# Performance work log

Hardware: AMD Instinct MI355X
Metric: run time of the kernel (lower is better)

The kernel has to match this reference:

```python
import jax, jax.numpy as jnp
import numpy as np

B, N, D = 2, 2048, 1024
H, DH = 16, 64
INNER = H * DH  # 1024
EPS = 1e-5


def setup_inputs() -> dict:
    key = jax.random.key(0)
    ks = jax.random.split(key, 7)
    x = jax.random.normal(ks[0], (B, N, D), dtype=jnp.float32)
    mask = jax.random.uniform(ks[1], (B, N)) < 0.9
    mask = mask.at[:, 0].set(True)  # guarantee at least one valid key per row
    attn_bias = jax.random.normal(ks[2], (H, N, N), dtype=jnp.float32) * 0.02
    ln_w = jnp.ones((D,), dtype=jnp.float32)
    ln_b = jnp.zeros((D,), dtype=jnp.float32)
    wq = jax.random.normal(ks[3], (D, INNER), dtype=jnp.float32) * 0.02
    wkv = jax.random.normal(ks[4], (D, 2 * DH), dtype=jnp.float32) * 0.02
    wo = jax.random.normal(ks[5], (INNER, D), dtype=jnp.float32) * 0.02
    return {"x": x, "attn_bias": attn_bias, "ln_w": ln_w, "ln_b": ln_b,
            "wq": wq, "wkv": wkv, "wo": wo, "mask": mask}


def reference(x, attn_bias, ln_w, ln_b, wq, wkv, wo, mask):
    scale = DH ** -0.5
    # NOTE: in the torch module, kv_input = x BEFORE self.norm (context=None),
    # so K/V come from raw x while Q comes from LayerNorm(x).
    mu = jnp.mean(x, axis=-1, keepdims=True)
    var = jnp.var(x, axis=-1, keepdims=True)
    xn = (x - mu) / jnp.sqrt(var + EPS) * ln_w + ln_b
    q = (xn @ wq).reshape(B, N, H, DH).transpose(0, 2, 1, 3) * scale  # b h n d
    kv = x @ wkv                     # b n 2*dh (shared single KV head, MQA)
    k, v = kv[..., :DH], kv[..., DH:]
    sim = jnp.einsum('bhid,bjd->bhij', q, k) + attn_bias  # bias broadcasts over b
    mask_value = -jnp.finfo(sim.dtype).max
    sim = jnp.where(mask[:, None, None, :], sim, mask_value)
    attn = jax.nn.softmax(sim, axis=-1)
    out = jnp.einsum('bhij,bjd->bhid', attn, v)
    out = out.transpose(0, 2, 1, 3).reshape(B, N, INNER)
    return out @ wo
```

## Files before the change

### kernel.cpp

```cpp
#include <hip/hip_runtime.h>
#include <hip/hip_bf16.h>

typedef __bf16 bf16_t;
typedef __bf16 bf16x4 __attribute__((ext_vector_type(4)));
typedef __bf16 bf16x8 __attribute__((ext_vector_type(8)));
typedef float f32x4 __attribute__((ext_vector_type(4)));

static constexpr int BB    = 2;
static constexpr int SEQ   = 2048;
static constexpr int DM    = 1024;
static constexpr int NHEAD = 16;
static constexpr int HD    = 64;
static constexpr float L2E = 1.4426950408889634f;

__device__ __forceinline__ bf16x8 ld8(const bf16_t* p) {
  return *reinterpret_cast<const bf16x8*>(p);
}

__device__ __forceinline__ void gl_lds16(const bf16_t* g, bf16_t* l) {
  __builtin_amdgcn_global_load_lds(
      (const __attribute__((address_space(1))) void*)g,
      (__attribute__((address_space(3))) void*)l, 16, 0, 0);
}

__device__ __forceinline__ uint2 shfl2(uint2 v, int src) {
  uint2 r;
  r.x = (unsigned)__shfl((int)v.x, src, 64);
  r.y = (unsigned)__shfl((int)v.y, src, 64);
  return r;
}

template <typename T> __device__ __forceinline__ T cvt_out(float v);
template <> __device__ __forceinline__ float  cvt_out<float >(float v) { return v; }
template <> __device__ __forceinline__ bf16_t cvt_out<bf16_t>(float v) { return (bf16_t)v; }

__global__ __launch_bounds__(256) void transpose_cast(const float* __restrict__ in,
                                                      bf16_t* __restrict__ out,
                                                      int R, int C) {
  __shared__ float tile[32][33];
  const int c0 = blockIdx.x * 32, r0 = blockIdx.y * 32;
  const int tx = threadIdx.x & 31, ty = threadIdx.x >> 5;
#pragma unroll
  for (int y = ty; y < 32; y += 8)
    tile[y][tx] = in[(size_t)(r0 + y) * C + (c0 + tx)];
  __syncthreads();
#pragma unroll
  for (int y = ty; y < 32; y += 8)
    out[(size_t)(c0 + y) * R + (r0 + tx)] = (bf16_t)tile[tx][y];
}

__global__ __launch_bounds__(256) void row_prep(const float* __restrict__ x,
    const float* __restrict__ ln_w, const float* __restrict__ ln_b,
    const int* __restrict__ mask,
    bf16_t* __restrict__ xbf, bf16_t* __restrict__ xn, float* __restrict__ maskA) {
  const int row = blockIdx.x, t = threadIdx.x;
  __shared__ float red[8];
  const float4 xv = *reinterpret_cast<const float4*>(&x[(size_t)row * DM + t * 4]);
  float s  = xv.x + xv.y + xv.z + xv.w;
  float s2 = xv.x * xv.x + xv.y * xv.y + xv.z * xv.z + xv.w * xv.w;
#pragma unroll
  for (int off = 32; off >= 1; off >>= 1) {
    s  += __shfl_xor(s,  off, 64);
    s2 += __shfl_xor(s2, off, 64);
  }
  if ((t & 63) == 0) { red[t >> 6] = s; red[4 + (t >> 6)] = s2; }
  __syncthreads();
  s  = red[0] + red[1] + red[2] + red[3];
  s2 = red[4] + red[5] + red[6] + red[7];
  const float mu   = s * (1.0f / DM);
  const float var  = s2 * (1.0f / DM) - mu * mu;
  const float rstd = rsqrtf(var + 1e-5f);
  const float4 wv = *reinterpret_cast<const float4*>(&ln_w[t * 4]);
  const float4 bv = *reinterpret_cast<const float4*>(&ln_b[t * 4]);
  union { bf16_t h[4]; uint2 u; } p0, p1;
  p0.h[0] = (bf16_t)xv.x; p0.h[1] = (bf16_t)xv.y;
  p0.h[2] = (bf16_t)xv.z; p0.h[3] = (bf16_t)xv.w;
  p1.h[0] = (bf16_t)((xv.x - mu) * rstd * wv.x + bv.x);
  p1.h[1] = (bf16_t)((xv.y - mu) * rstd * wv.y + bv.y);
  p1.h[2] = (bf16_t)((xv.z - mu) * rstd * wv.z + bv.z);
  p1.h[3] = (bf16_t)((xv.w - mu) * rstd * wv.w + bv.w);
  *reinterpret_cast<uint2*>(&xbf[(size_t)row * DM + t * 4]) = p0.u;
  *reinterpret_cast<uint2*>(&xn [(size_t)row * DM + t * 4]) = p1.u;
  if (t == 0) maskA[row] = mask[row] ? 0.0f : -1e30f;
}

__device__ __forceinline__ void gemm_core_db(
    const bf16_t* __restrict__ A, const bf16_t* __restrict__ Bt, int K,
    int m0, int n0, bf16_t* As, bf16_t* Bs, f32x4 (&acc)[4][4]) {
  const int t = threadIdx.x, lane = t & 63, w = t >> 6;
  const int wm = (w & 1) * 64, wn = (w >> 1) * 64;
  const int l15 = lane & 15, q4 = lane >> 4;
  const int sr = lane >> 2, sc = (lane & 3) * 8;
  const bf16_t* Ap0 = A  + (size_t)(m0 + w * 32 + sr) * K + sc;
  const bf16_t* Ap1 = Ap0 + (size_t)16 * K;
  const bf16_t* Bp0 = Bt + (size_t)(n0 + w * 32 + sr) * K + sc;
  const bf16_t* Bp1 = Bp0 + (size_t)16 * K;
  const int la0 = (w * 32) * 32, la1 = (w * 32 + 16) * 32;
  gl_lds16(Ap0, As + la0);
  gl_lds16(Ap1, As + la1);
  gl_lds16(Bp0, Bs + la0);
  gl_lds16(Bp1, Bs + la1);
  __syncthreads();
  int buf = 0;
  for (int k0 = 0; k0 < K; k0 += 32) {
    const int nbuf = buf ^ 1;
    if (k0 + 32 < K) {
      const int kn = k0 + 32;
      gl_lds16(Ap0 + kn, As + nbuf * (128 * 32) + la0);
      gl_lds16(Ap1 + kn, As + nbuf * (128 * 32) + la1);
      gl_lds16(Bp0 + kn, Bs + nbuf * (128 * 32) + la0);
      gl_lds16(Bp1 + kn, Bs + nbuf * (128 * 32) + la1);
    }
    const bf16_t* Asb = As + buf * (128 * 32);
    const bf16_t* Bsb = Bs + buf * (128 * 32);
    bf16x8 af[4], bfr[4];
#pragma unroll
    for (int mt = 0; mt < 4; ++mt) af[mt]  = ld8(&Asb[(wm + mt * 16 + l15) * 32 + q4 * 8]);
#pragma unroll
    for (int nt = 0; nt < 4; ++nt) bfr[nt] = ld8(&Bsb[(wn + nt * 16 + l15) * 32 + q4 * 8]);
#pragma unroll
    for (int mt = 0; mt < 4; ++mt)
#pragma unroll
      for (int nt = 0; nt < 4; ++nt)
        acc[mt][nt] = __builtin_amdgcn_mfma_f32_16x16x32_bf16(af[mt], bfr[nt], acc[mt][nt], 0, 0, 0);
    __syncthreads();
    buf = nbuf;
  }
}

__global__ __launch_bounds__(256) void gemm_qkv(
    const bf16_t* __restrict__ xn,  const bf16_t* __restrict__ wqT,  bf16_t* __restrict__ qb,
    const bf16_t* __restrict__ xbf, const bf16_t* __restrict__ wkvT,
    bf16_t* __restrict__ kkb, bf16_t* __restrict__ vTb) {
  __shared__ alignas(16) bf16_t As[2][128 * 32];
  __shared__ alignas(16) bf16_t Bs[2][128 * 32];
  const int bx = blockIdx.x;
  const bool isKV = (bx < 32);
  const int m0 = isKV ? bx * 128 : ((bx - 32) & 31) * 128;
  const int n0 = isKV ? 0 : ((bx - 32) >> 5) * 128;
  const bf16_t* A  = isKV ? xbf  : xn;
  const bf16_t* Bt = isKV ? wkvT : wqT;
  f32x4 acc[4][4] = {};
  gemm_core_db(A, Bt, DM, m0, n0, &As[0][0], &Bs[0][0], acc);

  const int lane = threadIdx.x & 63, w = threadIdx.x >> 6;
  const int wm = (w & 1) * 64, wn = (w >> 1) * 64;
  const int l15 = lane & 15, q4 = lane >> 4;
#pragma unroll
  for (int mt = 0; mt < 4; ++mt)
#pragma unroll
    for (int nt = 0; nt < 4; ++nt)
#pragma unroll
      for (int r = 0; r < 4; ++r) {
        const int gm = m0 + wm + mt * 16 + q4 * 4 + r;
        const int gn = n0 + wn + nt * 16 + l15;
        if (isKV) {
          const bf16_t ov = (bf16_t)acc[mt][nt][r];
          if (gn < HD) kkb[(size_t)gm * HD + gn] = ov;
          else vTb[((size_t)(gm >> 11) * HD + (gn - HD)) * SEQ + (gm & 2047)] = ov;
        } else {
          qb[(size_t)gm * DM + gn] = (bf16_t)(acc[mt][nt][r] * 0.125f);
        }
      }
}

__global__ __launch_bounds__(256) void gemm_out(const bf16_t* __restrict__ A,
    const bf16_t* __restrict__ Bt, float* __restrict__ C, int K) {
  __shared__ alignas(16) bf16_t As[2][128 * 32];
  __shared__ alignas(16) bf16_t Bs[2][128 * 32];
  const int m0 = blockIdx.x * 128, n0 = blockIdx.y * 128;
  f32x4 acc[4][4] = {};
  gemm_core_db(A, Bt, K, m0, n0, &As[0][0], &Bs[0][0], acc);
  const int lane = threadIdx.x & 63, w = threadIdx.x >> 6;
  const int wm = (w & 1) * 64, wn = (w >> 1) * 64;
  const int l15 = lane & 15, q4 = lane >> 4;
#pragma unroll
  for (int mt = 0; mt < 4; ++mt)
#pragma unroll
    for (int nt = 0; nt < 4; ++nt)
#pragma unroll
      for (int r = 0; r < 4; ++r) {
        const int gm = m0 + wm + mt * 16 + q4 * 4 + r;
        const int gn = n0 + wn + nt * 16 + l15;
        C[(size_t)gm * DM + gn] = acc[mt][nt][r];
      }
}

__global__ __launch_bounds__(256, 4) void flash_attn(
    const bf16_t* __restrict__ q,
    const bf16_t* __restrict__ kk,
    const bf16_t* __restrict__ vT,
    const float*  __restrict__ bias,
    const float*  __restrict__ maskA,
    bf16_t* __restrict__ aout)
{
  const int b = blockIdx.y & 1, h = blockIdx.y >> 1;
  const int i0 = blockIdx.x * 64;
  const int t = threadIdx.x, lane = t & 63, w = t >> 6;
  const int l15 = lane & 15, q4 = lane >> 4;

  __shared__ alignas(16) bf16_t Ks[2][64][72];
  __shared__ alignas(16) bf16_t Vs[2][64][72];

  const bf16_t* qrow = &q[((size_t)b * SEQ + i0 + w * 16 + l15) * DM + h * HD];
  const bf16x8 bq0 = ld8(qrow + q4 * 8);
  const bf16x8 bq1 = ld8(qrow + 32 + q4 * 8);

  f32x4 o[4] = {};
  float m_run = -1e30f, l_run = 0.0f;

  const float* bias_p = bias + (size_t)h * SEQ * SEQ
                      + (size_t)(i0 + w * 16 + l15) * SEQ + q4 * 4;
  const float* mask_p = maskA + b * SEQ + q4 * 4;

  const int sr = t >> 2, sc = (t & 3) * 16;
  const bf16_t* kp = &kk[((size_t)b * SEQ + sr) * HD + sc];
  const bf16_t* vp = &vT[((size_t)b * HD + sr) * SEQ + sc];

  uint4 kr0 = *reinterpret_cast<const uint4*>(kp);
  uint4 kr1 = *reinterpret_cast<const uint4*>(kp + 8);
  uint4 vr0 = *reinterpret_cast<const uint4*>(vp);
  uint4 vr1 = *reinterpret_cast<const uint4*>(vp + 8);
  f32x4 bm[4];
#pragma unroll
  for (int mt = 0; mt < 4; ++mt) {
    const f32x4 bv = *reinterpret_cast<const f32x4*>(bias_p + mt * 16);
    const f32x4 mv = *reinterpret_cast<const f32x4*>(mask_p + mt * 16);
    bm[mt] = bv + mv;
  }
  *reinterpret_cast<uint4*>(&Ks[0][sr][sc])     = kr0;
  *reinterpret_cast<uint4*>(&Ks[0][sr][sc + 8]) = kr1;
  *reinterpret_cast<uint4*>(&Vs[0][sr][sc])     = vr0;
  *reinterpret_cast<uint4*>(&Vs[0][sr][sc + 8]) = vr1;
  __syncthreads();

  for (int it = 0; it < SEQ / 64; ++it) {
    const int buf = it & 1;
    const int j1 = (it + 1) * 64;
    const bool more = (j1 < SEQ);
    if (more) {
      kr0 = *reinterpret_cast<const uint4*>(kp + (size_t)j1 * HD);
      kr1 = *reinterpret_cast<const uint4*>(kp + (size_t)j1 * HD + 8);
      vr0 = *reinterpret_cast<const uint4*>(vp + j1);
      vr1 = *reinterpret_cast<const uint4*>(vp + j1 + 8);
    }

    f32x4 s[4];
    __builtin_amdgcn_s_setprio(1);
#pragma unroll
    for (int mt = 0; mt < 4; ++mt) {
      const bf16x8 a0 = ld8(&Ks[buf][mt * 16 + l15][q4 * 8]);
      const bf16x8 a1 = ld8(&Ks[buf][mt * 16 + l15][32 + q4 * 8]);
      f32x4 z = {0.f, 0.f, 0.f, 0.f};
      z = __builtin_amdgcn_mfma_f32_16x16x32_bf16(a0, bq0, z, 0, 0, 0);
      z = __builtin_amdgcn_mfma_f32_16x16x32_bf16(a1, bq1, z, 0, 0, 0);
      s[mt] = z;
    }
    __builtin_amdgcn_s_setprio(0);

    float mx = -1e30f;
#pragma unroll
    for (int mt = 0; mt < 4; ++mt)
#pragma unroll
      for (int r = 0; r < 4; ++r) {
        s[mt][r] = s[mt][r] + bm[mt][r];
        mx = fmaxf(mx, s[mt][r]);
      }
    if (more) {
#pragma unroll
      for (int mt = 0; mt < 4; ++mt) {
        const f32x4 bv = *reinterpret_cast<const f32x4*>(bias_p + j1 + mt * 16);
        const f32x4 mv = *reinterpret_cast<const f32x4*>(mask_p + j1 + mt * 16);
        bm[mt] = bv + mv;
      }
    }
    mx = fmaxf(mx, __shfl_xor(mx, 16, 64));
    mx = fmaxf(mx, __shfl_xor(mx, 32, 64));
    const float mnew  = fmaxf(m_run, mx);
    const float alpha = __builtin_amdgcn_exp2f((m_run - mnew) * L2E);
    const float cc    = -mnew * L2E;
    m_run = mnew;

    float su = 0.0f;
#pragma unroll
    for (int mt = 0; mt < 4; ++mt)
#pragma unroll
      for (int r = 0; r < 4; ++r) {
        s[mt][r] = __builtin_amdgcn_exp2f(__builtin_fmaf(s[mt][r], L2E, cc));
        su += s[mt][r];
      }
    su += __shfl_xor(su, 16, 64);
    su += __shfl_xor(su, 32, 64);
    l_run = l_run * alpha + su;

#pragma unroll
    for (int r = 0; r < 4; ++r) {
      const float a_r = __shfl(alpha, q4 * 4 + r, 64);
      o[0][r] *= a_r; o[1][r] *= a_r; o[2][r] *= a_r; o[3][r] *= a_r;
    }

    uint2 pk[4];
#pragma unroll
    for (int mt = 0; mt < 4; ++mt) {
      union { bf16_t hh[4]; uint2 u; } pu;
      pu.hh[0] = (bf16_t)s[mt][0]; pu.hh[1] = (bf16_t)s[mt][1];
      pu.hh[2] = (bf16_t)s[mt][2]; pu.hh[3] = (bf16_t)s[mt][3];
      pk[mt] = pu.u;
    }
    const int src0 = ((q4 & 1) << 5) + l15;
    const int src1 = src0 + 16;
    const bool hiSel = (q4 >> 1) != 0;
#pragma unroll
    for (int ks = 0; ks < 2; ++ks) {
      const uint2 a0 = shfl2(pk[2 * ks],     src0);
      const uint2 a1 = shfl2(pk[2 * ks + 1], src0);
      const uint2 b0 = shfl2(pk[2 * ks],     src1);
      const uint2 b1 = shfl2(pk[2 * ks + 1], src1);
      union { unsigned u[4]; bf16x8 v; } pf;
      pf.u[0] = hiSel ? a1.x : a0.x; pf.u[1] = hiSel ? a1.y : a0.y;
      pf.u[2] = hiSel ? b1.x : b0.x; pf.u[3] = hiSel ? b1.y : b0.y;
      __builtin_amdgcn_s_setprio(1);
#pragma unroll
      for (int nt = 0; nt < 4; ++nt) {
        const bf16x8 vv = ld8(&Vs[buf][nt * 16 + l15][ks * 32 + q4 * 8]);
        o[nt] = __builtin_amdgcn_mfma_f32_16x16x32_bf16(pf.v, vv, o[nt], 0, 0, 0);
      }
      __builtin_amdgcn_s_setprio(0);
    }

    if (more) {
      *reinterpret_cast<uint4*>(&Ks[buf ^ 1][sr][sc])     = kr0;
      *reinterpret_cast<uint4*>(&Ks[buf ^ 1][sr][sc + 8]) = kr1;
      *reinterpret_cast<uint4*>(&Vs[buf ^ 1][sr][sc])     = vr0;
      *reinterpret_cast<uint4*>(&Vs[buf ^ 1][sr][sc + 8]) = vr1;
    }
    __syncthreads();
  }

#pragma unroll
  for (int r = 0; r < 4; ++r) {
    const float linv = 1.0f / __shfl(l_run, q4 * 4 + r, 64);
    const int gi = i0 + w * 16 + q4 * 4 + r;
    bf16_t* dst = &aout[((size_t)b * SEQ + gi) * DM + h * HD];
#pragma unroll
    for (int nt = 0; nt < 4; ++nt)
      dst[nt * 16 + l15] = (bf16_t)(o[nt][r] * linv);
  }
}

extern "C" void kernel_launch(void* const* d_in, const int* in_sizes, int n_in,
                              void* d_out, int out_size, void* d_ws, size_t ws_size,
                              hipStream_t stream) {
  const float* x         = (const float*)d_in[0];
  const float* attn_bias = (const float*)d_in[1];
  const float* ln_w      = (const float*)d_in[2];
  const float* ln_b      = (const float*)d_in[3];
  const float* wq        = (const float*)d_in[4];
  const float* wkv       = (const float*)d_in[5];
  const float* wo        = (const float*)d_in[6];
  const int*   mask      = (const int*)d_in[7];
  float* out = (float*)d_out;

  char* ws = (char*)d_ws;
  size_t off = 0;
  auto alloc = [&](size_t bytes) {
    char* p = ws + off;
    off += (bytes + 255) & ~(size_t)255;
    return p;
  };
  bf16_t* xbf   = (bf16_t*)alloc((size_t)BB * SEQ * DM * 2);
  bf16_t* xn    = (bf16_t*)alloc((size_t)BB * SEQ * DM * 2);
  bf16_t* wqT   = (bf16_t*)alloc((size_t)DM * DM * 2);
  bf16_t* wkvT  = (bf16_t*)alloc((size_t)2 * HD * DM * 2);
  bf16_t* woT   = (bf16_t*)alloc((size_t)DM * DM * 2);
  bf16_t* qb    = (bf16_t*)alloc((size_t)BB * SEQ * DM * 2);
  bf16_t* kkb   = (bf16_t*)alloc((size_t)BB * SEQ * HD * 2);
  bf16_t* vTb   = (bf16_t*)alloc((size_t)BB * HD * SEQ * 2);
  bf16_t* aoutb = (bf16_t*)alloc((size_t)BB * SEQ * DM * 2);
  float*  maskA = (float*)alloc((size_t)BB * SEQ * 4);

  transpose_cast<<<dim3(DM / 32, DM / 32), 256, 0, stream>>>(wq, wqT, DM, DM);
  transpose_cast<<<dim3(128 / 32, DM / 32), 256, 0, stream>>>(wkv, wkvT, DM, 128);
  transpose_cast<<<dim3(DM / 32, DM / 32), 256, 0, stream>>>(wo, woT, DM, DM);
  row_prep<<<BB * SEQ, 256, 0, stream>>>(x, ln_w, ln_b, mask, xbf, xn, maskA);
  gemm_qkv<<<288, 256, 0, stream>>>(xn, wqT, qb, xbf, wkvT, kkb, vTb);
  flash_attn<<<dim3(SEQ / 64, BB * NHEAD), 256, 0, stream>>>(qb, kkb, vTb, attn_bias,
                                                             maskA, aoutb);
  gemm_out<<<dim3(32, 8), 256, 0, stream>>>(aoutb, woT, out, DM);
}
```

Before: 527.6 us.

## Merge prep kernels into one launch and drop setprio in attention

Fuses the three weight transpose-cast launches and the row LayerNorm prep into a single prep_all kernel that dispatches on block index, saving three kernel launches and their tail gaps. Separately, the flash attention loop removes the s_setprio hints around its MFMA sections. It also keeps bias and mask as separate register arrays and adds them at use time instead of pre-summing them. The GEMM k-loop is pinned to no unrolling. These changes shift register pressure and scheduling in the attention kernel, and the effect on instruction interleaving is uncertain.

```diff
diff --git a/kernel.cpp b/kernel.cpp
--- a/kernel.cpp
+++ b/kernel.cpp
@@ -34,11 +34,11 @@
 template <> __device__ __forceinline__ float  cvt_out<float >(float v) { return v; }
 template <> __device__ __forceinline__ bf16_t cvt_out<bf16_t>(float v) { return (bf16_t)v; }
 
-__global__ __launch_bounds__(256) void transpose_cast(const float* __restrict__ in,
-                                                      bf16_t* __restrict__ out,
-                                                      int R, int C) {
-  __shared__ float tile[32][33];
-  const int c0 = blockIdx.x * 32, r0 = blockIdx.y * 32;
+__device__ __forceinline__ void tc_body(const float* __restrict__ in,
+                                        bf16_t* __restrict__ out,
+                                        int R, int C, int bx, int by,
+                                        float (*tile)[33]) {
+  const int c0 = bx * 32, r0 = by * 32;
   const int tx = threadIdx.x & 31, ty = threadIdx.x >> 5;
 #pragma unroll
   for (int y = ty; y < 32; y += 8)
@@ -49,12 +49,12 @@
     out[(size_t)(c0 + y) * R + (r0 + tx)] = (bf16_t)tile[tx][y];
 }
 
-__global__ __launch_bounds__(256) void row_prep(const float* __restrict__ x,
-    const float* __restrict__ ln_w, const float* __restrict__ ln_b,
-    const int* __restrict__ mask,
-    bf16_t* __restrict__ xbf, bf16_t* __restrict__ xn, float* __restrict__ maskA) {
-  const int row = blockIdx.x, t = threadIdx.x;
-  __shared__ float red[8];
+__device__ __forceinline__ void row_prep_body(int row,
+    const float* __restrict__ x, const float* __restrict__ ln_w,
+    const float* __restrict__ ln_b, const int* __restrict__ mask,
+    bf16_t* __restrict__ xbf, bf16_t* __restrict__ xn, float* __restrict__ maskA,
+    float* red) {
+  const int t = threadIdx.x;
   const float4 xv = *reinterpret_cast<const float4*>(&x[(size_t)row * DM + t * 4]);
   float s  = xv.x + xv.y + xv.z + xv.w;
   float s2 = xv.x * xv.x + xv.y * xv.y + xv.z * xv.z + xv.w * xv.w;
@@ -84,6 +84,29 @@
   if (t == 0) maskA[row] = mask[row] ? 0.0f : -1e30f;
 }
 
+__global__ __launch_bounds__(256) void prep_all(
+    const float* __restrict__ x, const float* __restrict__ ln_w,
+    const float* __restrict__ ln_b, const int* __restrict__ mask,
+    const float* __restrict__ wq, const float* __restrict__ wkv,
+    const float* __restrict__ wo,
+    bf16_t* __restrict__ xbf, bf16_t* __restrict__ xn, float* __restrict__ maskA,
+    bf16_t* __restrict__ wqT, bf16_t* __restrict__ wkvT, bf16_t* __restrict__ woT) {
+  __shared__ float tile[32][33];
+  __shared__ float red[8];
+  const int bid = blockIdx.x;
+  if (bid < 1024) {
+    tc_body(wq, wqT, DM, DM, bid & 31, bid >> 5, tile);
+  } else if (bid < 1152) {
+    const int id = bid - 1024;
+    tc_body(wkv, wkvT, DM, 128, id & 3, id >> 2, tile);
+  } else if (bid < 2176) {
+    const int id = bid - 1152;
+    tc_body(wo, woT, DM, DM, id & 31, id >> 5, tile);
+  } else {
+    row_prep_body(bid - 2176, x, ln_w, ln_b, mask, xbf, xn, maskA, red);
+  }
+}
+
 __device__ __forceinline__ void gemm_core_db(
     const bf16_t* __restrict__ A, const bf16_t* __restrict__ Bt, int K,
     int m0, int n0, bf16_t* As, bf16_t* Bs, f32x4 (&acc)[4][4]) {
@@ -102,6 +125,7 @@
   gl_lds16(Bp1, Bs + la1);
   __syncthreads();
   int buf = 0;
+#pragma unroll 1
   for (int k0 = 0; k0 < K; k0 += 32) {
     const int nbuf = buf ^ 1;
     if (k0 + 32 < K) {
@@ -221,12 +245,11 @@
   uint4 kr1 = *reinterpret_cast<const uint4*>(kp + 8);
   uint4 vr0 = *reinterpret_cast<const uint4*>(vp);
   uint4 vr1 = *reinterpret_cast<const uint4*>(vp + 8);
-  f32x4 bm[4];
+  f32x4 bv[4], mv[4];
 #pragma unroll
   for (int mt = 0; mt < 4; ++mt) {
-    const f32x4 bv = *reinterpret_cast<const f32x4*>(bias_p + mt * 16);
-    const f32x4 mv = *reinterpret_cast<const f32x4*>(mask_p + mt * 16);
-    bm[mt] = bv + mv;
+    bv[mt] = *reinterpret_cast<const f32x4*>(bias_p + mt * 16);
+    mv[mt] = *reinterpret_cast<const f32x4*>(mask_p + mt * 16);
   }
   *reinterpret_cast<uint4*>(&Ks[0][sr][sc])     = kr0;
   *reinterpret_cast<uint4*>(&Ks[0][sr][sc + 8]) = kr1;
@@ -246,7 +269,6 @@
     }
 
     f32x4 s[4];
-    __builtin_amdgcn_s_setprio(1);
 #pragma unroll
     for (int mt = 0; mt < 4; ++mt) {
       const bf16x8 a0 = ld8(&Ks[buf][mt * 16 + l15][q4 * 8]);
@@ -256,22 +278,20 @@
       z = __builtin_amdgcn_mfma_f32_16x16x32_bf16(a1, bq1, z, 0, 0, 0);
       s[mt] = z;
     }
-    __builtin_amdgcn_s_setprio(0);
 
     float mx = -1e30f;
 #pragma unroll
     for (int mt = 0; mt < 4; ++mt)
 #pragma unroll
       for (int r = 0; r < 4; ++r) {
-        s[mt][r] = s[mt][r] + bm[mt][r];
+        s[mt][r] = s[mt][r] + bv[mt][r] + mv[mt][r];
         mx = fmaxf(mx, s[mt][r]);
       }
     if (more) {
 #pragma unroll
       for (int mt = 0; mt < 4; ++mt) {
-        const f32x4 bv = *reinterpret_cast<const f32x4*>(bias_p + j1 + mt * 16);
-        const f32x4 mv = *reinterpret_cast<const f32x4*>(mask_p + j1 + mt * 16);
-        bm[mt] = bv + mv;
+        bv[mt] = *reinterpret_cast<const f32x4*>(bias_p + j1 + mt * 16);
+        mv[mt] = *reinterpret_cast<const f32x4*>(mask_p + j1 + mt * 16);
       }
     }
     mx = fmaxf(mx, __shfl_xor(mx, 16, 64));
@@ -319,13 +339,11 @@
       union { unsigned u[4]; bf16x8 v; } pf;
       pf.u[0] = hiSel ? a1.x : a0.x; pf.u[1] = hiSel ? a1.y : a0.y;
       pf.u[2] = hiSel ? b1.x : b0.x; pf.u[3] = hiSel ? b1.y : b0.y;
-      __builtin_amdgcn_s_setprio(1);
 #pragma unroll
       for (int nt = 0; nt < 4; ++nt) {
         const bf16x8 vv = ld8(&Vs[buf][nt * 16 + l15][ks * 32 + q4 * 8]);
         o[nt] = __builtin_amdgcn_mfma_f32_16x16x32_bf16(pf.v, vv, o[nt], 0, 0, 0);
       }
-      __builtin_amdgcn_s_setprio(0);
     }
 
     if (more) {
@@ -379,10 +397,8 @@
   bf16_t* aoutb = (bf16_t*)alloc((size_t)BB * SEQ * DM * 2);
   float*  maskA = (float*)alloc((size_t)BB * SEQ * 4);
 
-  transpose_cast<<<dim3(DM / 32, DM / 32), 256, 0, stream>>>(wq, wqT, DM, DM);
-  transpose_cast<<<dim3(128 / 32, DM / 32), 256, 0, stream>>>(wkv, wkvT, DM, 128);
-  transpose_cast<<<dim3(DM / 32, DM / 32), 256, 0, stream>>>(wo, woT, DM, DM);
-  row_prep<<<BB * SEQ, 256, 0, stream>>>(x, ln_w, ln_b, mask, xbf, xn, maskA);
+  prep_all<<<6272, 256, 0, stream>>>(x, ln_w, ln_b, mask, wq, wkv, wo,
+                                     xbf, xn, maskA, wqT, wkvT, woT);
   gemm_qkv<<<288, 256, 0, stream>>>(xn, wqT, qb, xbf, wkvT, kkb, vTb);
   flash_attn<<<dim3(SEQ / 64, BB * NHEAD), 256, 0, stream>>>(qb, kkb, vTb, attn_bias,
                                                              maskA, aoutb);
```

Result: faster. 479.3 us (-9.2%).
